# Kernel tuning notes

Measured on AMD Instinct MI355X. Metric: run time of the kernel, lower is better.

Reference implementation:

```python
import jax, jax.numpy as jnp
import numpy as np

N = 50000      # nodes
E = 800000     # edges (before self-loops)
IN = 64        # in_dim
C = 64         # hidden_dim (per-head out channels)
H = 4          # heads
NEG_SLOPE = 0.2


def setup_inputs() -> dict:
    key = jax.random.key(0)
    ks = jax.random.split(key, 9)
    x = jax.random.normal(ks[0], (N, IN), jnp.float32)
    edge_index = jax.random.randint(ks[1], (2, E), 0, N)
    edge_attr = jax.random.uniform(ks[2], (E, 1), jnp.float32)
    s_in = 1.0 / np.sqrt(IN)
    s_c = 1.0 / np.sqrt(C)
    W = jax.random.normal(ks[3], (IN, H * C), jnp.float32) * s_in
    att_src = jax.random.normal(ks[4], (H, C), jnp.float32) * s_c
    att_dst = jax.random.normal(ks[5], (H, C), jnp.float32) * s_c
    lin_edge_w = jax.random.normal(ks[6], (1, H * C), jnp.float32)
    att_edge = jax.random.normal(ks[7], (H, C), jnp.float32) * s_c
    bias = jnp.zeros((C,), jnp.float32)
    return dict(x=x, edge_index=edge_index, edge_attr=edge_attr, W=W,
                att_src=att_src, att_dst=att_dst, lin_edge_w=lin_edge_w,
                att_edge=att_edge, bias=bias)


def reference(x, edge_index, edge_attr, W, att_src, att_dst, lin_edge_w, att_edge, bias):
    n = x.shape[0]
    # add self-loops (PyG default add_self_loops=True, fill_value='mean')
    loop = jnp.arange(n)
    src = jnp.concatenate([edge_index[0], loop])          # [E+N]
    dst = jnp.concatenate([edge_index[1], loop])          # [E+N]
    ea = jnp.concatenate([edge_attr,
                          jnp.full((n, 1), edge_attr.mean(), edge_attr.dtype)], axis=0)
    # node transform: [N, H, C]
    h = (x @ W).reshape(n, H, C)
    a_src = jnp.einsum('nhc,hc->nh', h, att_src)          # [N, H]
    a_dst = jnp.einsum('nhc,hc->nh', h, att_dst)          # [N, H]
    eh = (ea @ lin_edge_w).reshape(-1, H, C)              # [E+N, H, C]
    a_edge = jnp.einsum('ehc,hc->eh', eh, att_edge)       # [E+N, H]
    # per-edge attention logit
    alpha = a_src[src] + a_dst[dst] + a_edge              # [E+N, H]
    alpha = jax.nn.leaky_relu(alpha, NEG_SLOPE)
    # segment softmax over edges grouped by destination node
    amax = jax.ops.segment_max(alpha, dst, num_segments=n)
    alpha = jnp.exp(alpha - amax[dst])
    asum = jax.ops.segment_sum(alpha, dst, num_segments=n)
    alpha = alpha / (asum[dst] + 1e-16)                   # [E+N, H]
    # weighted message + scatter-add aggregation
    msg = h[src] * alpha[..., None]                       # [E+N, H, C]
    out = jax.ops.segment_sum(msg, dst, num_segments=n)   # [N, H, C]
    out = out.mean(axis=1) + bias                         # concat=False -> head mean
    # ReLU + residual
    return jax.nn.relu(out) + x
```

## Files before the change

### kernel.cpp

```cpp
#include <hip/hip_runtime.h>
#include <hip/hip_fp16.h>
#include <math.h>

#define H 4
#define C 64
#define HC 256
#define NEG 0.2f
#define ROWU 64
#define MAXREC 63
#define XPAD 72
#define HPAD 264
#define BKT 128
#define BSH 7
#define ARN 2816
#define TILE 8192

typedef __attribute__((ext_vector_type(8))) _Float16 half8;
typedef __attribute__((ext_vector_type(4))) float f32x4;
typedef float f32x2 __attribute__((vector_size(8)));

__global__ __launch_bounds__(256) void phase1_kernel(
    const float* __restrict__ x, const float* __restrict__ W,
    const float* __restrict__ att_src, const float* __restrict__ att_dst,
    const int* __restrict__ ei, const float* __restrict__ edge_attr,
    unsigned char* __restrict__ h, float* __restrict__ a_src, float* __restrict__ a_dst,
    uint2* __restrict__ arena, unsigned* __restrict__ cursor,
    float* __restrict__ mean_acc, int Nn, int Ee, int G1, int G2) {
    int t = threadIdx.x;
    if ((int)blockIdx.x < G1) {
        __shared__ __align__(16) _Float16 xs[16 * XPAD];
        __shared__ __align__(16) _Float16 hs[16 * HPAD];
        int w = t >> 6, lane = t & 63, quad = lane >> 4, c16 = lane & 15;
        half8 bf[4][2];
#pragma unroll
        for (int nt = 0; nt < 4; ++nt)
#pragma unroll
            for (int kh = 0; kh < 2; ++kh)
#pragma unroll
                for (int j = 0; j < 8; ++j)
                    bf[nt][kh][j] = (_Float16)W[(kh * 32 + quad * 8 + j) * HC +
                                                w * 64 + nt * 16 + c16];
        float ats[4], atd[4];
#pragma unroll
        for (int nt = 0; nt < 4; ++nt) {
            ats[nt] = att_src[w * 64 + nt * 16 + c16];
            atd[nt] = att_dst[w * 64 + nt * 16 + c16];
        }

        int nTiles = (Nn + 15) >> 4;
        for (int mt = blockIdx.x; mt < nTiles; mt += G1) {
            __syncthreads();
            {
                int row = t >> 4, col4 = (t & 15) * 4;
                int node = mt * 16 + row;
                float4 v = make_float4(0.f, 0.f, 0.f, 0.f);
                if (node < Nn) v = *(const float4*)(x + (size_t)node * 64 + col4);
                _Float16* dst = xs + row * XPAD + col4;
                dst[0] = (_Float16)v.x; dst[1] = (_Float16)v.y;
                dst[2] = (_Float16)v.z; dst[3] = (_Float16)v.w;
            }
            __syncthreads();
            half8 a0 = *(const half8*)(xs + c16 * XPAD + quad * 8);
            half8 a1 = *(const half8*)(xs + c16 * XPAD + 32 + quad * 8);
            f32x4 d[4];
#pragma unroll
            for (int nt = 0; nt < 4; ++nt) {
                f32x4 acc = {0.f, 0.f, 0.f, 0.f};
                acc = __builtin_amdgcn_mfma_f32_16x16x32_f16(a0, bf[nt][0], acc, 0, 0, 0);
                acc = __builtin_amdgcn_mfma_f32_16x16x32_f16(a1, bf[nt][1], acc, 0, 0, 0);
                d[nt] = acc;
            }
#pragma unroll
            for (int reg = 0; reg < 4; ++reg) {
                float ps = 0.f, pd = 0.f;
#pragma unroll
                for (int nt = 0; nt < 4; ++nt) {
                    ps += d[nt][reg] * ats[nt];
                    pd += d[nt][reg] * atd[nt];
                }
                ps += __shfl_xor(ps, 1); pd += __shfl_xor(pd, 1);
                ps += __shfl_xor(ps, 2); pd += __shfl_xor(pd, 2);
                ps += __shfl_xor(ps, 4); pd += __shfl_xor(pd, 4);
                ps += __shfl_xor(ps, 8); pd += __shfl_xor(pd, 8);
                if (c16 == 0) {
                    int node = mt * 16 + quad * 4 + reg;
                    if (node < Nn) {
                        a_src[node * 4 + w] = ps;
                        a_dst[node * 4 + w] = pd;
                    }
                }
            }
#pragma unroll
            for (int nt = 0; nt < 4; ++nt)
#pragma unroll
                for (int reg = 0; reg < 4; ++reg)
                    hs[(quad * 4 + reg) * HPAD + w * 64 + nt * 16 + c16] =
                        (_Float16)d[nt][reg];
            __syncthreads();
            {
                int row = t >> 4, chunk = t & 15;
                int node = mt * 16 + row;
                if (node < Nn) {
                    const uint4* sp = (const uint4*)(hs + row * HPAD + chunk * 16);
                    uint4 sA = sp[0], sB = sp[1];
                    unsigned ua[8] = {sA.x, sA.y, sA.z, sA.w, sB.x, sB.y, sB.z, sB.w};
                    unsigned ow[4];
#pragma unroll
                    for (int q = 0; q < 4; ++q) {
                        float2 p0 = __half22float2(*reinterpret_cast<const __half2*>(&ua[q * 2]));
                        float2 p1 = __half22float2(*reinterpret_cast<const __half2*>(&ua[q * 2 + 1]));
                        int v = __builtin_amdgcn_cvt_pk_fp8_f32(p0.x, p0.y, 0, false);
                        v = __builtin_amdgcn_cvt_pk_fp8_f32(p1.x, p1.y, v, true);
                        ow[q] = (unsigned)v;
                    }
                    *(uint4*)(h + (size_t)node * HC + chunk * 16) =
                        make_uint4(ow[0], ow[1], ow[2], ow[3]);
                }
            }
        }
    } else {
        __shared__ float red[256];
        __shared__ unsigned cntA[512], baseA[512];
        int nbkt = (Nn + BKT - 1) >> BSH;
        int ntile = (Ee + TILE - 1) / TILE;
        float s = 0.f;
        for (int tile = (int)blockIdx.x - G1; tile < ntile; tile += G2) {
            int e0 = tile * TILE;
            for (int bb = t; bb < nbkt; bb += 256) cntA[bb] = 0;
            __syncthreads();
#pragma unroll 4
            for (int k = 0; k < TILE / 256; ++k) {
                int i = e0 + k * 256 + t;
                if (i < Ee) {
                    int dst = ei[Ee + i];
                    s += edge_attr[i];
                    atomicAdd(&cntA[dst >> BSH], 1u);
                }
            }
            __syncthreads();
            for (int bb = t; bb < nbkt; bb += 256) {
                unsigned c = cntA[bb];
                baseA[bb] = c ? atomicAdd(&cursor[bb], c) : 0u;
                cntA[bb] = 0;
            }
            __syncthreads();
#pragma unroll 4
            for (int k = 0; k < TILE / 256; ++k) {
                int i = e0 + k * 256 + t;
                if (i < Ee) {
                    int src = ei[i];
                    int dst = ei[Ee + i];
                    float ea = edge_attr[i];
                    unsigned q = (unsigned)(ea * 65535.f + 0.5f);
                    int b = dst >> BSH;
                    unsigned r = atomicAdd(&cntA[b], 1u);
                    unsigned idx = baseA[b] + r;
                    if (idx < ARN)
                        arena[(size_t)b * ARN + idx] =
                            make_uint2((q << 16) | (unsigned)src,
                                       (unsigned)(dst & (BKT - 1)));
                }
            }
            __syncthreads();
        }
        red[t] = s;
        __syncthreads();
        for (int o = 128; o; o >>= 1) {
            if (t < o) red[t] += red[t + o];
            __syncthreads();
        }
        if (t == 0) atomicAdd(mean_acc, red[0]);
    }
}

__global__ __launch_bounds__(256) void bucket_kernel(
    const uint2* __restrict__ arena, const unsigned* __restrict__ cursor,
    unsigned* __restrict__ edges) {
    __shared__ unsigned rows[BKT * ROWU];
    __shared__ unsigned cnt[BKT];
    int b = blockIdx.x, t = threadIdx.x;
    if (t < BKT) cnt[t] = 0;
    __syncthreads();
    unsigned nb = cursor[b];
    if (nb > ARN) nb = ARN;
    for (unsigned i = t; i < nb; i += 256) {
        uint2 e = arena[(size_t)b * ARN + i];
        unsigned r = atomicAdd(&cnt[e.y], 1u);
        if (r < MAXREC) rows[e.y * ROWU + 1 + r] = e.x;
    }
    __syncthreads();
    if (t < BKT) rows[t * ROWU] = cnt[t] < (unsigned)MAXREC ? cnt[t] : (unsigned)MAXREC;
    __syncthreads();
    size_t obase = (size_t)b * (BKT * ROWU);
    for (int i = t; i < BKT * (ROWU / 4); i += 256)
        *(uint4*)(edges + obase + i * 4) = *(const uint4*)(rows + i * 4);
}

__global__ __launch_bounds__(256) void aggregate_kernel(
    const unsigned* __restrict__ edges,
    const float* __restrict__ a_src, const float* __restrict__ a_dst,
    const float* __restrict__ lin_edge_w, const float* __restrict__ att_edge,
    const float* __restrict__ mean_acc, const unsigned char* __restrict__ h,
    const float* __restrict__ bias, const float* __restrict__ x,
    float* __restrict__ out, int Nn, float invE) {
    int lane = threadIdx.x & 63;
    int n = blockIdx.x * 4 + (threadIdx.x >> 6);
    if (n >= Nn) return;
    int head = lane >> 4;

    size_t rowbase = (size_t)n * ROWU;
    unsigned deg = edges[rowbase];
    unsigned rec = edges[rowbase + 1 + lane];
    const unsigned* h8 = (const unsigned*)h;
    unsigned sv = h8[(size_t)n * 64 + lane];
    float mean = mean_acc[0] * invE;
    float ad = a_dst[n * 4 + head];
    float asn = a_src[n * 4 + head];

    int sub = lane & 15;
    float kp = 0.f;
#pragma unroll
    for (int j = 0; j < 4; ++j) {
        int c = sub * 4 + j;
        kp += lin_edge_w[head * C + c] * att_edge[head * C + c];
    }
    kp += __shfl_xor(kp, 1);
    kp += __shfl_xor(kp, 2);
    kp += __shfl_xor(kp, 4);
    kp += __shfl_xor(kp, 8);
    float K = kp;
    const float DEQ = 1.0f / 65535.f;

    if (deg > MAXREC) deg = MAXREC;

    float ls = asn + ad + mean * K;
    ls = ls > 0.f ? ls : NEG * ls;
    float wsl = __expf(ls);
    f32x2 s01 = __builtin_amdgcn_cvt_pk_f32_fp8((int)sv, false);
    f32x2 s23 = __builtin_amdgcn_cvt_pk_f32_fp8((int)sv, true);
    float4 acc = make_float4(wsl * s01[0], wsl * s01[1], wsl * s23[0], wsl * s23[1]);
    float swgt = wsl;

    int i = 0;
    for (; i + 4 <= (int)deg; i += 4) {
        unsigned r0 = (unsigned)__builtin_amdgcn_readlane((int)rec, i + 0);
        unsigned r1 = (unsigned)__builtin_amdgcn_readlane((int)rec, i + 1);
        unsigned r2 = (unsigned)__builtin_amdgcn_readlane((int)rec, i + 2);
        unsigned r3 = (unsigned)__builtin_amdgcn_readlane((int)rec, i + 3);
        int s0 = r0 & 0xFFFF, s1 = r1 & 0xFFFF, s2 = r2 & 0xFFFF, s3 = r3 & 0xFFFF;
        unsigned hv0 = h8[(size_t)s0 * 64 + lane];
        unsigned hv1 = h8[(size_t)s1 * 64 + lane];
        unsigned hv2 = h8[(size_t)s2 * 64 + lane];
        unsigned hv3 = h8[(size_t)s3 * 64 + lane];
        float l0 = a_src[s0 * 4 + head] + ad + (float)(r0 >> 16) * DEQ * K;
        float l1 = a_src[s1 * 4 + head] + ad + (float)(r1 >> 16) * DEQ * K;
        float l2 = a_src[s2 * 4 + head] + ad + (float)(r2 >> 16) * DEQ * K;
        float l3 = a_src[s3 * 4 + head] + ad + (float)(r3 >> 16) * DEQ * K;
        l0 = l0 > 0.f ? l0 : NEG * l0;
        l1 = l1 > 0.f ? l1 : NEG * l1;
        l2 = l2 > 0.f ? l2 : NEG * l2;
        l3 = l3 > 0.f ? l3 : NEG * l3;
        float w0 = __expf(l0), w1 = __expf(l1), w2 = __expf(l2), w3 = __expf(l3);
        swgt += (w0 + w1) + (w2 + w3);
        {
            f32x2 f01 = __builtin_amdgcn_cvt_pk_f32_fp8((int)hv0, false);
            f32x2 f23 = __builtin_amdgcn_cvt_pk_f32_fp8((int)hv0, true);
            acc.x += w0 * f01[0]; acc.y += w0 * f01[1];
            acc.z += w0 * f23[0]; acc.w += w0 * f23[1];
        }
        {
            f32x2 f01 = __builtin_amdgcn_cvt_pk_f32_fp8((int)hv1, false);
            f32x2 f23 = __builtin_amdgcn_cvt_pk_f32_fp8((int)hv1, true);
            acc.x += w1 * f01[0]; acc.y += w1 * f01[1];
            acc.z += w1 * f23[0]; acc.w += w1 * f23[1];
        }
        {
            f32x2 f01 = __builtin_amdgcn_cvt_pk_f32_fp8((int)hv2, false);
            f32x2 f23 = __builtin_amdgcn_cvt_pk_f32_fp8((int)hv2, true);
            acc.x += w2 * f01[0]; acc.y += w2 * f01[1];
            acc.z += w2 * f23[0]; acc.w += w2 * f23[1];
        }
        {
            f32x2 f01 = __builtin_amdgcn_cvt_pk_f32_fp8((int)hv3, false);
            f32x2 f23 = __builtin_amdgcn_cvt_pk_f32_fp8((int)hv3, true);
            acc.x += w3 * f01[0]; acc.y += w3 * f01[1];
            acc.z += w3 * f23[0]; acc.w += w3 * f23[1];
        }
    }
    for (; i < (int)deg; ++i) {
        unsigned r = (unsigned)__builtin_amdgcn_readlane((int)rec, i);
        int s0 = r & 0xFFFF;
        unsigned hv = h8[(size_t)s0 * 64 + lane];
        float l = a_src[s0 * 4 + head] + ad + (float)(r >> 16) * DEQ * K;
        l = l > 0.f ? l : NEG * l;
        float wg = __expf(l);
        swgt += wg;
        f32x2 f01 = __builtin_amdgcn_cvt_pk_f32_fp8((int)hv, false);
        f32x2 f23 = __builtin_amdgcn_cvt_pk_f32_fp8((int)hv, true);
        acc.x += wg * f01[0]; acc.y += wg * f01[1];
        acc.z += wg * f23[0]; acc.w += wg * f23[1];
    }

    float inv = 1.f / (swgt + 1e-16f);
    acc.x *= inv; acc.y *= inv; acc.z *= inv; acc.w *= inv;

    acc.x += __shfl_xor(acc.x, 16);
    acc.y += __shfl_xor(acc.y, 16);
    acc.z += __shfl_xor(acc.z, 16);
    acc.w += __shfl_xor(acc.w, 16);
    acc.x += __shfl_xor(acc.x, 32);
    acc.y += __shfl_xor(acc.y, 32);
    acc.z += __shfl_xor(acc.z, 32);
    acc.w += __shfl_xor(acc.w, 32);
    if (lane < 16) {
        float4 b = ((const float4*)bias)[lane];
        float4 xv = ((const float4*)x)[(size_t)n * 16 + lane];
        float4 o;
        o.x = fmaxf(acc.x * 0.25f + b.x, 0.f) + xv.x;
        o.y = fmaxf(acc.y * 0.25f + b.y, 0.f) + xv.y;
        o.z = fmaxf(acc.z * 0.25f + b.z, 0.f) + xv.z;
        o.w = fmaxf(acc.w * 0.25f + b.w, 0.f) + xv.w;
        ((float4*)out)[(size_t)n * 16 + lane] = o;
    }
}

extern "C" void kernel_launch(void* const* d_in, const int* in_sizes, int n_in,
                              void* d_out, int out_size, void* d_ws, size_t ws_size,
                              hipStream_t stream) {
    const float* x = (const float*)d_in[0];
    const int* ei = (const int*)d_in[1];
    const float* edge_attr = (const float*)d_in[2];
    const float* W = (const float*)d_in[3];
    const float* att_src = (const float*)d_in[4];
    const float* att_dst = (const float*)d_in[5];
    const float* lin_edge_w = (const float*)d_in[6];
    const float* att_edge = (const float*)d_in[7];
    const float* bias = (const float*)d_in[8];
    float* out = (float*)d_out;
    int Nn = in_sizes[0] / 64;
    int Ee = in_sizes[1] / 2;
    int NB = (Nn + BKT - 1) >> BSH;

    char* p = (char*)d_ws;
    size_t off = 0;
    auto alloc = [&](size_t bytes) -> char* {
        char* r = p + off;
        off += (bytes + 255) & ~(size_t)255;
        return r;
    };
    float* mean_acc = (float*)alloc(256);
    unsigned* cursor = (unsigned*)alloc((size_t)NB * 4);
    size_t zero_bytes = off;
    uint2* arena = (uint2*)alloc((size_t)NB * ARN * 8);
    unsigned* edges = (unsigned*)alloc((size_t)NB * BKT * ROWU * 4);
    unsigned char* h = (unsigned char*)alloc((size_t)Nn * HC);
    float* a_src = (float*)alloc((size_t)Nn * H * 4);
    float* a_dst = (float*)alloc((size_t)Nn * H * 4);
    (void)ws_size;

    int ntile = (Ee + TILE - 1) / TILE;
    const int G1 = 512;
    int G2 = ntile < 2048 ? ntile : 2048;
    hipMemsetAsync(d_ws, 0, zero_bytes, stream);
    phase1_kernel<<<G1 + G2, 256, 0, stream>>>(x, W, att_src, att_dst, ei, edge_attr,
                                               h, a_src, a_dst, arena, cursor,
                                               mean_acc, Nn, Ee, G1, G2);
    bucket_kernel<<<NB, 256, 0, stream>>>(arena, cursor, edges);
    aggregate_kernel<<<(Nn + 3) / 4, 256, 0, stream>>>(edges, a_src, a_dst,
                                                       lin_edge_w, att_edge, mean_acc,
                                                       h, bias, x, out, Nn,
                                                       1.0f / (float)Ee);
}
```

Before: 163.3 us.

## Replace global-cursor edge binning with per-tile fixed-size segments

The edge binning stage no longer does a counting pass plus global atomic cursor reservation per bucket. Instead each 2048-edge tile writes its edges into a private fixed 32-slot segment per destination bucket and records the per-tile counts, so only one pass over the edges is made and no global atomics are needed. The bucket kernel then scans every tile's segment for its bucket, using the counts to skip empty slots. In exchange, the bucket kernel reads a sparser arena laid out as ntile x SEG per bucket, and a bucket that gets more than 32 edges from one tile silently drops the extras.

```diff
diff --git a/kernel.cpp b/kernel.cpp
--- a/kernel.cpp
+++ b/kernel.cpp
@@ -12,8 +12,9 @@
 #define HPAD 264
 #define BKT 128
 #define BSH 7
-#define ARN 2816
-#define TILE 8192
+#define TILE 2048
+#define SEG 32
+#define SEGSH 5
 
 typedef __attribute__((ext_vector_type(8))) _Float16 half8;
 typedef __attribute__((ext_vector_type(4))) float f32x4;
@@ -24,8 +25,8 @@
     const float* __restrict__ att_src, const float* __restrict__ att_dst,
     const int* __restrict__ ei, const float* __restrict__ edge_attr,
     unsigned char* __restrict__ h, float* __restrict__ a_src, float* __restrict__ a_dst,
-    uint2* __restrict__ arena, unsigned* __restrict__ cursor,
-    float* __restrict__ mean_acc, int Nn, int Ee, int G1, int G2) {
+    uint2* __restrict__ arena, unsigned* __restrict__ counts,
+    float* __restrict__ mean_acc, int Nn, int Ee, int G1, int ntile) {
     int t = threadIdx.x;
     if ((int)blockIdx.x < G1) {
         __shared__ __align__(16) _Float16 xs[16 * XPAD];
@@ -120,48 +121,34 @@
         }
     } else {
         __shared__ float red[256];
-        __shared__ unsigned cntA[512], baseA[512];
+        __shared__ unsigned cntA[512];
         int nbkt = (Nn + BKT - 1) >> BSH;
-        int ntile = (Ee + TILE - 1) / TILE;
+        int tile = (int)blockIdx.x - G1;
+        for (int bb = t; bb < nbkt; bb += 256) cntA[bb] = 0;
+        __syncthreads();
+        int e0 = tile * TILE;
         float s = 0.f;
-        for (int tile = (int)blockIdx.x - G1; tile < ntile; tile += G2) {
-            int e0 = tile * TILE;
-            for (int bb = t; bb < nbkt; bb += 256) cntA[bb] = 0;
-            __syncthreads();
 #pragma unroll 4
-            for (int k = 0; k < TILE / 256; ++k) {
-                int i = e0 + k * 256 + t;
-                if (i < Ee) {
-                    int dst = ei[Ee + i];
-                    s += edge_attr[i];
-                    atomicAdd(&cntA[dst >> BSH], 1u);
-                }
-            }
-            __syncthreads();
-            for (int bb = t; bb < nbkt; bb += 256) {
-                unsigned c = cntA[bb];
-                baseA[bb] = c ? atomicAdd(&cursor[bb], c) : 0u;
-                cntA[bb] = 0;
-            }
-            __syncthreads();
-#pragma unroll 4
-            for (int k = 0; k < TILE / 256; ++k) {
-                int i = e0 + k * 256 + t;
-                if (i < Ee) {
-                    int src = ei[i];
-                    int dst = ei[Ee + i];
-                    float ea = edge_attr[i];
-                    unsigned q = (unsigned)(ea * 65535.f + 0.5f);
-                    int b = dst >> BSH;
-                    unsigned r = atomicAdd(&cntA[b], 1u);
-                    unsigned idx = baseA[b] + r;
-                    if (idx < ARN)
-                        arena[(size_t)b * ARN + idx] =
-                            make_uint2((q << 16) | (unsigned)src,
-                                       (unsigned)(dst & (BKT - 1)));
-                }
-            }
-            __syncthreads();
+        for (int k = 0; k < TILE / 256; ++k) {
+            int i = e0 + k * 256 + t;
+            if (i < Ee) {
+                int src = ei[i];
+                int dst = ei[Ee + i];
+                float ea = edge_attr[i];
+                s += ea;
+                unsigned q = (unsigned)(ea * 65535.f + 0.5f);
+                int b = dst >> BSH;
+                unsigned r = atomicAdd(&cntA[b], 1u);
+                if (r < SEG)
+                    arena[((size_t)b * ntile + tile) * SEG + r] =
+                        make_uint2((q << 16) | (unsigned)src,
+                                   (unsigned)(dst & (BKT - 1)));
+            }
+        }
+        __syncthreads();
+        for (int bb = t; bb < nbkt; bb += 256) {
+            unsigned c = cntA[bb];
+            counts[(size_t)bb * ntile + tile] = c < (unsigned)SEG ? c : (unsigned)SEG;
         }
         red[t] = s;
         __syncthreads();
@@ -174,19 +161,25 @@
 }
 
 __global__ __launch_bounds__(256) void bucket_kernel(
-    const uint2* __restrict__ arena, const unsigned* __restrict__ cursor,
-    unsigned* __restrict__ edges) {
+    const uint2* __restrict__ arena, const unsigned* __restrict__ counts,
+    unsigned* __restrict__ edges, int ntile) {
     __shared__ unsigned rows[BKT * ROWU];
     __shared__ unsigned cnt[BKT];
+    __shared__ unsigned short segc[512];
     int b = blockIdx.x, t = threadIdx.x;
     if (t < BKT) cnt[t] = 0;
+    for (int j = t; j < ntile; j += 256)
+        segc[j] = (unsigned short)counts[(size_t)b * ntile + j];
     __syncthreads();
-    unsigned nb = cursor[b];
-    if (nb > ARN) nb = ARN;
-    for (unsigned i = t; i < nb; i += 256) {
-        uint2 e = arena[(size_t)b * ARN + i];
-        unsigned r = atomicAdd(&cnt[e.y], 1u);
-        if (r < MAXREC) rows[e.y * ROWU + 1 + r] = e.x;
+    int total = ntile * SEG;
+    size_t base = (size_t)b * ntile * SEG;
+    for (int j = t; j < total; j += 256) {
+        int seg = j >> SEGSH, slot = j & (SEG - 1);
+        if (slot < (int)segc[seg]) {
+            uint2 e = arena[base + j];
+            unsigned r = atomicAdd(&cnt[e.y], 1u);
+            if (r < MAXREC) rows[e.y * ROWU + 1 + r] = e.x;
+        }
     }
     __syncthreads();
     if (t < BKT) rows[t * ROWU] = cnt[t] < (unsigned)MAXREC ? cnt[t] : (unsigned)MAXREC;
@@ -340,6 +333,7 @@
     int Nn = in_sizes[0] / 64;
     int Ee = in_sizes[1] / 2;
     int NB = (Nn + BKT - 1) >> BSH;
+    int ntile = (Ee + TILE - 1) / TILE;
 
     char* p = (char*)d_ws;
     size_t off = 0;
@@ -349,23 +343,21 @@
         return r;
     };
     float* mean_acc = (float*)alloc(256);
-    unsigned* cursor = (unsigned*)alloc((size_t)NB * 4);
     size_t zero_bytes = off;
-    uint2* arena = (uint2*)alloc((size_t)NB * ARN * 8);
+    unsigned* counts = (unsigned*)alloc((size_t)NB * ntile * 4);
+    uint2* arena = (uint2*)alloc((size_t)NB * ntile * SEG * 8);
     unsigned* edges = (unsigned*)alloc((size_t)NB * BKT * ROWU * 4);
     unsigned char* h = (unsigned char*)alloc((size_t)Nn * HC);
     float* a_src = (float*)alloc((size_t)Nn * H * 4);
     float* a_dst = (float*)alloc((size_t)Nn * H * 4);
     (void)ws_size;
 
-    int ntile = (Ee + TILE - 1) / TILE;
     const int G1 = 512;
-    int G2 = ntile < 2048 ? ntile : 2048;
     hipMemsetAsync(d_ws, 0, zero_bytes, stream);
-    phase1_kernel<<<G1 + G2, 256, 0, stream>>>(x, W, att_src, att_dst, ei, edge_attr,
-                                               h, a_src, a_dst, arena, cursor,
-                                               mean_acc, Nn, Ee, G1, G2);
-    bucket_kernel<<<NB, 256, 0, stream>>>(arena, cursor, edges);
+    phase1_kernel<<<G1 + ntile, 256, 0, stream>>>(x, W, att_src, att_dst, ei, edge_attr,
+                                                  h, a_src, a_dst, arena, counts,
+                                                  mean_acc, Nn, Ee, G1, ntile);
+    bucket_kernel<<<NB, 256, 0, stream>>>(arena, counts, edges, ntile);
     aggregate_kernel<<<(Nn + 3) / 4, 256, 0, stream>>>(edges, a_src, a_dst,
                                                        lin_edge_w, att_edge, mean_acc,
                                                        h, bias, x, out, Nn,
```

Result: no change. 164.1 us (+0.5%).
